# Optimization experiments

Measured on AMD Instinct MI355X. Metric: run time of the kernel, lower is better.

The kernel has to match this reference:

```python
import jax, jax.numpy as jnp
import numpy as np

# hidden irreps: 16x0e + 8x1o (dim 40); key/query: 8x0e + 4x1o (dim 24)
M0, M1 = 16, 8
K0, K1 = 8, 4
NB, HID = 16, 64       # radial basis size, radial MLP hidden
MAX_R = 2.0
NLAYERS = 2
SQ3 = 3.0 ** 0.5
N_NODES, N_EDGES = 8192, 131072


def _split(x, m0, m1):
    # [N, m0 + 3*m1] -> scalars [N,m0], vectors [N,m1,3]
    return x[:, :m0], x[:, m0:m0 + 3 * m1].reshape(x.shape[0], m1, 3)


def _lin(x, W0, W1, m0, m1):
    # e3nn o3.Linear: per-l block matmul with 1/sqrt(fan_in) norm
    s, v = _split(x, m0, m1)
    so = (s @ W0) * (m0 ** -0.5)
    vo = jnp.einsum('nui,uw->nwi', v, W1) * (m1 ** -0.5)
    return jnp.concatenate([so, vo.reshape(x.shape[0], -1)], axis=1)


def _radial(emb, W1, W2):
    # e3nn FullyConnectedNet [NB -> HID -> numel], no bias, 1/sqrt(fan_in)
    h = jax.nn.silu((emb @ W1) * (NB ** -0.5))
    return (h @ W2) * (HID ** -0.5)


def _fctp(s, v, y1, w, mo0, mo1):
    # FullyConnectedTensorProduct (hidden x sh(0e+1o) -> mo0 x0e + mo1 x1o)
    # with per-edge weights w. Y_0 = 1 under 'component' normalization.
    # Paths (in order of the weight slices):
    #   0e x 0e -> 0e,  0e x 1o -> 1o,  1o x 0e -> 1o,  1o x 1o -> 0e
    En, m0 = s.shape
    m1 = v.shape[1]
    i = 0
    W1 = w[:, i:i + m0 * mo0].reshape(En, m0, mo0); i += m0 * mo0
    W2 = w[:, i:i + m0 * mo1].reshape(En, m0, mo1); i += m0 * mo1
    W3 = w[:, i:i + m1 * mo1].reshape(En, m1, mo1); i += m1 * mo1
    W4 = w[:, i:i + m1 * mo0].reshape(En, m1, mo0)
    fan = float(m0 + m1)  # total mul1*mul2 feeding each output irrep
    vy = jnp.einsum('eui,ei->eu', v, y1) / SQ3  # w3j(1,1,0) = delta/sqrt3
    out_s = (jnp.einsum('eu,euw->ew', s, W1)
             + jnp.einsum('eu,euw->ew', vy, W4)) * (fan ** -0.5)
    out_v = (jnp.einsum('eu,ek,euw->ewk', s, y1, W2) / SQ3
             + jnp.einsum('eui,euw->ewi', v, W3)) * (SQ3 * fan ** -0.5)
    return out_s, out_v


def _edge_embed(d):
    # soft_one_hot_linspace(basis='gaussian', cutoff=True) * sqrt(NB)
    vals = jnp.linspace(0.0, MAX_R, NB + 2)[1:-1]
    step = MAX_R / (NB + 1)
    diff = (d[:, None] - vals) / step
    return (jnp.exp(-diff * diff) / 1.12) * (NB ** 0.5)


def _soft_unit_step(x):
    xs = jnp.maximum(x, 1e-9)
    return jnp.where(x > 0.0, jnp.exp(-1.0 / xs), 0.0)


def _layer(x, pos, src, dst, hq0, hq1, fck1, fck2, fcv1, fcv2, dot0, dot1):
    Nn = x.shape[0]
    vec = pos[src] - pos[dst]
    d = jnp.sqrt(jnp.sum(vec * vec, -1) + 1e-24)
    emb = _edge_embed(d)
    cutoff = _soft_unit_step(10.0 * (1.0 - d / MAX_R))
    y1 = SQ3 * vec / d[:, None]  # l=1 spherical harmonic, 'component' norm
    q = _lin(x, hq0, hq1, M0, M1)
    fs, fv = _split(x[src], M0, M1)
    ks_, kv_ = _fctp(fs, fv, y1, _radial(emb, fck1, fck2), K0, K1)
    vs_, vv_ = _fctp(fs, fv, y1, _radial(emb, fcv1, fcv2), M0, M1)
    qs, qv = _split(q[dst], K0, K1)
    fan = float(K0 * K0 + K1 * K1)
    logits = (jnp.einsum('eu,ev,uv->e', qs, ks_, dot0)
              + jnp.einsum('eui,evi,uv->e', qv, kv_, dot1) / SQ3) * (fan ** -0.5)
    mx = jax.ops.segment_max(logits, dst, num_segments=Nn)
    mx = jnp.where(jnp.isfinite(mx), mx, 0.0)
    ex = cutoff * jnp.exp(logits - mx[dst])
    z = jax.ops.segment_sum(ex, dst, num_segments=Nn)
    z = jnp.where(z == 0.0, 1.0, z)
    alpha = ex / z[dst]
    wgt = jnp.sqrt(jax.nn.relu(alpha) + 1e-12)
    val = jnp.concatenate([vs_, vv_.reshape(vs_.shape[0], -1)], axis=1)
    return jax.ops.segment_sum(wgt[:, None] * val, dst, num_segments=Nn)


def setup_inputs() -> dict:
    key = jax.random.key(0)
    ks = jax.random.split(key, 20)
    rn = lambda k, s: jax.random.normal(k, s, jnp.float32)
    f = rn(ks[0], (N_NODES, 40))
    pos = jax.random.uniform(ks[1], (N_NODES, 3), jnp.float32)
    src = jax.random.randint(ks[2], (N_EDGES,), 0, N_NODES, jnp.int32)
    off = jax.random.randint(ks[3], (N_EDGES,), 1, N_NODES, jnp.int32)
    dst = ((src + off) % N_NODES).astype(jnp.int32)  # no self-loops (loop=False)
    L = NLAYERS
    return dict(
        f=f, pos=pos,
        lin_in0=rn(ks[4], (16, 16)), lin_in1=rn(ks[5], (8, 8)),
        hq0=rn(ks[6], (L, 16, 8)), hq1=rn(ks[7], (L, 8, 4)),
        fck1=rn(ks[8], (L, 16, 64)), fck2=rn(ks[9], (L, 64, 288)),
        fcv1=rn(ks[10], (L, 16, 64)), fcv2=rn(ks[11], (L, 64, 576)),
        dot0=rn(ks[12], (L, 8, 8)), dot1=rn(ks[13], (L, 4, 4)),
        rb0=rn(ks[14], (16, 8)), rb1=rn(ks[15], (8, 4)),
        re0=rn(ks[16], (16, 8)), re1=rn(ks[17], (8, 4)),
        edge_src=src, edge_dst=dst,
    )


def reference(f, pos, lin_in0, lin_in1, hq0, hq1, fck1, fck2, fcv1, fcv2,
              dot0, dot1, rb0, rb1, re0, re1, edge_src, edge_dst):
    x = _lin(f, lin_in0, lin_in1, M0, M1)
    for l in range(NLAYERS):
        x = x + _layer(x, pos, edge_src, edge_dst, hq0[l], hq1[l],
                       fck1[l], fck2[l], fcv1[l], fcv2[l], dot0[l], dot1[l])
    b = _lin(x, rb0, rb1, M0, M1)
    eta = _lin(x, re0, re1, M0, M1)
    return b, eta
```

## Files before the change

### kernel.cpp

```cpp
#include <hip/hip_runtime.h>
#include <hip/hip_bf16.h>
#include <math.h>

#define DEV __device__ __forceinline__

typedef __attribute__((ext_vector_type(4))) float f32x4;
typedef __attribute__((ext_vector_type(8))) __bf16 bf16x8;

constexpr int N_CONST = 8192;
constexpr int E_CONST = 131072;

constexpr float SQ3F     = 1.7320508075688772f;
constexpr float INV_SQ3F = 0.57735026918962576f;
constexpr float FAN_TP   = 0.20412414523193150f;
constexpr float FAN_TP_V = 0.35355339059327373f;
constexpr float FAN_DOT  = 0.11180339887498949f;
constexpr float INV16SQ  = 0.25f;
constexpr float INV8SQ   = 0.35355339059327373f;
constexpr float HID_SC   = 0.125f;

enum : int {
  OFF_LIN0 = 0,
  OFF_LIN1 = OFF_LIN0 + 256,
  OFF_HQ0  = OFF_LIN1 + 64,
  OFF_HQ1  = OFF_HQ0 + 256,
  OFF_FCK1 = OFF_HQ1 + 64,
  OFF_FCK2 = OFF_FCK1 + 2048,
  OFF_FCV1 = OFF_FCK2 + 36864,
  OFF_FCV2 = OFF_FCV1 + 2048,
  OFF_DOT0 = OFF_FCV2 + 73728,
  OFF_DOT1 = OFF_DOT0 + 128,
  OFF_RB0  = OFF_DOT1 + 32,
  OFF_RB1  = OFF_RB0 + 128,
  OFF_RE0  = OFF_RB1 + 32,
  OFF_RE1  = OFF_RE0 + 128,
  OFF_F    = OFF_RE1 + 32,
  OFF_POS  = OFF_F + N_CONST * 40,
  OFF_X    = OFF_POS + N_CONST * 3,
  OFF_Q    = OFF_X + N_CONST * 40,
  OFF_MX   = OFF_Q + N_CONST * 20,
  OFF_Z    = OFF_MX + N_CONST,
  OFF_AGG  = OFF_Z + N_CONST,
  OFF_LOGIT= OFF_AGG + N_CONST * 40,
  OFF_CUT  = OFF_LOGIT + E_CONST,
  OFF_EX   = OFF_CUT + E_CONST,
  OFF_FLAG = OFF_EX + E_CONST,
  OFF_WT   = (OFF_FLAG + 7) & ~3,
  OFF_WTK  = OFF_WT + 36864,
};

__global__ void k_detect(const unsigned int* __restrict__ words, int* __restrict__ flag) {
  if (blockIdx.x != 0 || threadIdx.x != 0) return;
  int cnt = 0;
  for (int i = 0; i < 512; ++i) {
    unsigned b = (words[i] >> 8) & 0x7Fu;
    cnt += (b >= 0x3Au && b <= 0x43u) ? 1 : 0;
  }
  *flag = (cnt > 256) ? 1 : 0;
}

struct CvtArgs {
  const void* src[16];
  int n[16];
  int off[16];
};

template <bool BF>
__global__ void k_cvt(CvtArgs a, float* __restrict__ ws, const int* __restrict__ flag) {
  if ((*flag != 0) != BF) return;
  int tid = blockIdx.x * blockDim.x + threadIdx.x;
  int stride = gridDim.x * blockDim.x;
  for (int arr = 0; arr < 16; ++arr) {
    float* dst = ws + a.off[arr];
    int n = a.n[arr];
    if (BF) {
      const __hip_bfloat16* s = (const __hip_bfloat16*)a.src[arr];
      for (int i = tid; i < n; i += stride) dst[i] = __bfloat162float(s[i]);
    } else {
      const float* s = (const float*)a.src[arr];
      for (int i = tid; i < n; i += stride) dst[i] = s[i];
    }
  }
}

DEV unsigned short f2bf(float f) {
  unsigned int u = __float_as_uint(f);
  u = u + 0x7FFFu + ((u >> 16) & 1u);
  return (unsigned short)(u >> 16);
}

DEV void atomicMaxF(float* addr, float val) {
  unsigned int* ai = (unsigned int*)addr;
  unsigned int old = *ai;
  while (__uint_as_float(old) < val) {
    unsigned int assumed = old;
    old = atomicCAS(ai, assumed, __float_as_uint(val));
    if (old == assumed) break;
  }
}

template <int MO0, int MO1>
DEV void lin_apply(const float* __restrict__ in40, const float* __restrict__ W0,
                   const float* __restrict__ W1, float* __restrict__ out) {
#pragma unroll
  for (int j = 0; j < MO0; ++j) {
    float a = 0.f;
#pragma unroll
    for (int i = 0; i < 16; ++i) a += in40[i] * W0[i * MO0 + j];
    out[j] = a * INV16SQ;
  }
#pragma unroll
  for (int w = 0; w < MO1; ++w) {
    float a0 = 0.f, a1 = 0.f, a2 = 0.f;
#pragma unroll
    for (int u = 0; u < 8; ++u) {
      float wt = W1[u * MO1 + w];
      a0 += in40[16 + u * 3 + 0] * wt;
      a1 += in40[16 + u * 3 + 1] * wt;
      a2 += in40[16 + u * 3 + 2] * wt;
    }
    out[MO0 + w * 3 + 0] = a0 * INV8SQ;
    out[MO0 + w * 3 + 1] = a1 * INV8SQ;
    out[MO0 + w * 3 + 2] = a2 * INV8SQ;
  }
}

DEV void edge_emb(float d, float emb[16]) {
#pragma unroll
  for (int i = 0; i < 16; ++i) {
    float c = (2.0f * (i + 1)) / 17.0f;
    float df = (d - c) * (17.0f * 0.5f);
    emb[i] = __expf(-df * df) * (4.0f / 1.12f);
  }
}

DEV void radial_hidden16(const float* __restrict__ W1, const float emb[16],
                         int wv, float h[16]) {
#pragma unroll 1
  for (int i = 0; i < 16; ++i) {
    float a = 0.f;
#pragma unroll
    for (int j = 0; j < 16; ++j) a += emb[j] * W1[j * 64 + wv * 16 + i];
    a *= INV16SQ;
    float sig = 1.0f / (1.0f + __expf(-a));
    h[i] = a * sig * HID_SC;
  }
}

DEV void pack16(unsigned short* __restrict__ dst, const float h[16]) {
  unsigned int hw[8];
#pragma unroll
  for (int i = 0; i < 8; ++i)
    hw[i] = (unsigned int)f2bf(h[2 * i]) | ((unsigned int)f2bf(h[2 * i + 1]) << 16);
  uint4 w0 = {hw[0], hw[1], hw[2], hw[3]};
  uint4 w1 = {hw[4], hw[5], hw[6], hw[7]};
  *(uint4*)(dst) = w0;
  *(uint4*)(dst + 8) = w1;
}

DEV f32x4 gemm2_lds(const unsigned short* __restrict__ wb, int c, int g,
                    bf16x8 a0, bf16x8 a1) {
  const f32x4 zero4 = {0.f, 0.f, 0.f, 0.f};
  int s0 = g ^ (c & 7);
  bf16x8 b0 = __builtin_bit_cast(bf16x8, *(const uint4*)(wb + c * 64 + s0 * 8));
  bf16x8 b1 = __builtin_bit_cast(bf16x8, *(const uint4*)(wb + c * 64 + (s0 ^ 4) * 8));
  f32x4 acc = __builtin_amdgcn_mfma_f32_16x16x32_bf16(a0, b0, zero4, 0, 0, 0);
  return __builtin_amdgcn_mfma_f32_16x16x32_bf16(a1, b1, acc, 0, 0, 0);
}

__global__ void k_wt(const float* __restrict__ fcv2, unsigned short* __restrict__ wt) {
  int tid = blockIdx.x * blockDim.x + threadIdx.x;
  if (tid >= 2 * 36864) return;
  int l = tid / 36864;
  int r = tid - l * 36864;
  int T = r >> 10;
  int w = r & 1023;
  int c = w >> 6;
  int q = w & 63;
  int slot = (q >> 3) ^ (c & 7);
  int k = slot * 8 + (q & 7);
  wt[tid] = f2bf(fcv2[l * 36864 + k * 576 + T * 16 + c]);
}

__global__ void k_wtk(const float* __restrict__ fck2, unsigned short* __restrict__ wtk) {
  int tid = blockIdx.x * blockDim.x + threadIdx.x;
  if (tid >= 2 * 18432) return;
  int l = tid / 18432;
  int r = tid - l * 18432;
  int T = r >> 10;
  int w = r & 1023;
  int c = w >> 6;
  int q = w & 63;
  int slot = (q >> 3) ^ (c & 7);
  int k = slot * 8 + (q & 7);
  wtk[tid] = f2bf(fck2[l * 18432 + k * 288 + T * 16 + c]);
}

__global__ void k_lin_in(const float* __restrict__ f, const float* __restrict__ W0,
                         const float* __restrict__ W1, float* __restrict__ x, int N) {
  int n = blockIdx.x * blockDim.x + threadIdx.x;
  if (n >= N) return;
  lin_apply<16, 8>(f + n * 40, W0, W1, x + n * 40);
}

__global__ void k_q(const float* __restrict__ x, const float* __restrict__ W0,
                    const float* __restrict__ W1, float* __restrict__ q, int N) {
  int n = blockIdx.x * blockDim.x + threadIdx.x;
  if (n >= N) return;
  lin_apply<8, 4>(x + n * 40, W0, W1, q + n * 20);
}

__global__ void k_init(float* __restrict__ mx, float* __restrict__ z,
                       float* __restrict__ agg, int N) {
  int i = blockIdx.x * blockDim.x + threadIdx.x;
  if (i < N * 40) agg[i] = 0.f;
  if (i < N) { mx[i] = -INFINITY; z[i] = 0.f; }
}

__global__ void k_update(float* __restrict__ x, const float* __restrict__ agg, int n) {
  int i = blockIdx.x * blockDim.x + threadIdx.x;
  if (i < n) x[i] += agg[i];
}

__global__ void k_edge_ex(const int* __restrict__ dstv, const float* __restrict__ logit,
                          const float* __restrict__ cutb, const float* __restrict__ mx,
                          float* __restrict__ ex, float* __restrict__ z, int E) {
  int e = blockIdx.x * blockDim.x + threadIdx.x;
  if (e >= E) return;
  int t = dstv[e];
  float m = mx[t];
  if (m == -INFINITY) m = 0.f;
  float v = cutb[e] * __expf(logit[e] - m);
  ex[e] = v;
  atomicAdd(&z[t], v);
}

__global__ void __launch_bounds__(256)
k_edge_k(const float* __restrict__ pos, const float* __restrict__ x,
         const float* __restrict__ q,
         const float* __restrict__ fck1, const unsigned short* __restrict__ wtk,
         const float* __restrict__ dot0, const float* __restrict__ dot1,
         const int* __restrict__ srcv, const int* __restrict__ dstv,
         float* __restrict__ logit, float* __restrict__ cutb,
         float* __restrict__ mx, int E) {
  __shared__ alignas(16) unsigned short h_lds[64 * 72];
  __shared__ alignas(16) unsigned short wbuf[2 * 2 * 1024];
  __shared__ float fS[48][64];
  __shared__ float y1A[64][4];
  __shared__ float qdA[64][8];
  __shared__ float qvA[64][12];
  __shared__ int dstA[64];

  const int tid = threadIdx.x;
  const int wv = __builtin_amdgcn_readfirstlane(tid >> 6);
  const int lane = tid & 63;
  const int e0 = blockIdx.x * 64;
  const int eL = e0 + lane;
  const bool valid = eL < E;
  const bool ldr = (wv < 2);

  uint4 pre0, pre1;
  if (ldr) {
    const unsigned short* gs = wtk + wv * 1024 + lane * 8;
    pre0 = *(const uint4*)(gs);
    pre1 = *(const uint4*)(gs + 512);
  }

  int s = valid ? srcv[eL] : 0, t = valid ? dstv[eL] : 0;

  float y1v[3], d;
  {
    float vx = pos[s * 3 + 0] - pos[t * 3 + 0];
    float vy_ = pos[s * 3 + 1] - pos[t * 3 + 1];
    float vz = pos[s * 3 + 2] - pos[t * 3 + 2];
    d = sqrtf(vx * vx + vy_ * vy_ + vz * vz + 1e-24f);
    float inv = SQ3F / d;
    y1v[0] = vx * inv; y1v[1] = vy_ * inv; y1v[2] = vz * inv;
  }
  float emb[16];
  edge_emb(d, emb);
  {
    float h[16];
    radial_hidden16(fck1, emb, wv, h);
    pack16(&h_lds[lane * 72 + 16 * wv], h);
  }

  if (wv == 0) {
    const float* xs = x + s * 40;
    float fvl[24];
#pragma unroll
    for (int i = 0; i < 16; ++i) fS[i][lane] = xs[i];
#pragma unroll
    for (int i = 0; i < 24; ++i) { fvl[i] = xs[16 + i]; fS[16 + i][lane] = fvl[i]; }
#pragma unroll
    for (int u = 0; u < 8; ++u)
      fS[40 + u][lane] = (fvl[u * 3] * y1v[0] + fvl[u * 3 + 1] * y1v[1] +
                          fvl[u * 3 + 2] * y1v[2]) * INV_SQ3F;
    y1A[lane][0] = y1v[0]; y1A[lane][1] = y1v[1]; y1A[lane][2] = y1v[2];
    dstA[lane] = t;
    if (valid) {
      float uu = 10.0f * (1.0f - 0.5f * d);
      cutb[eL] = (uu > 0.f) ? __expf(-1.0f / fmaxf(uu, 1e-9f)) : 0.f;
    }
    const float* qd_ = q + t * 20;
    float qs_[8], qv_[12];
#pragma unroll
    for (int u = 0; u < 8; ++u) qs_[u] = qd_[u];
#pragma unroll
    for (int i = 0; i < 12; ++i) qv_[i] = qd_[8 + i];
#pragma unroll
    for (int v = 0; v < 8; ++v) {
      float a = 0.f;
#pragma unroll
      for (int u = 0; u < 8; ++u) a += qs_[u] * dot0[u * 8 + v];
      qdA[lane][v] = a * (FAN_DOT * FAN_TP);
    }
#pragma unroll
    for (int v = 0; v < 4; ++v)
#pragma unroll
      for (int i = 0; i < 3; ++i) {
        float a = 0.f;
#pragma unroll
        for (int u = 0; u < 4; ++u) a += qv_[u * 3 + i] * dot1[u * 4 + v];
        qvA[lane][v * 3 + i] = a * (FAN_DOT * INV_SQ3F);
      }
  }
  if (ldr) {
    unsigned short* wd = wbuf + wv * 1024 + lane * 8;
    *(uint4*)(wd) = pre0;
    *(uint4*)(wd + 512) = pre1;
  }
  __syncthreads();

  const int c = lane & 15, g = lane >> 4;
  const int erow = 16 * wv + 4 * g;

  bf16x8 a0 = __builtin_bit_cast(bf16x8, *(const uint4*)&h_lds[(16 * wv + c) * 72 + 8 * g]);
  bf16x8 a1 = __builtin_bit_cast(bf16x8, *(const uint4*)&h_lds[(16 * wv + c) * 72 + 32 + 8 * g]);

  float ksp[4] = {0.f, 0.f, 0.f, 0.f};
  float a2p[4] = {0.f, 0.f, 0.f, 0.f};
  float a3p[4][3] = {{0.f}};

#pragma unroll 1
  for (int p = 0; p < 9; ++p) {
    uint4 nb0, nb1;
    const bool hasNext = (p < 8) && ldr;
    if (hasNext) {
      const unsigned short* gs = wtk + (2 * (p + 1) + wv) * 1024 + lane * 8;
      nb0 = *(const uint4*)(gs);
      nb1 = *(const uint4*)(gs + 512);
    }
    const unsigned short* wb = wbuf + (p & 1) * 2048;
#pragma unroll
    for (int t2 = 0; t2 < 2; ++t2) {
      int T = 2 * p + t2;
      f32x4 acc = gemm2_lds(wb + t2 * 1024, c, g, a0, a1);
      if (T < 8) {
        int u = 2 * T + (c >> 3);
#pragma unroll
        for (int j = 0; j < 4; ++j) ksp[j] += fS[u][erow + j] * acc[j];
      } else if (T < 12) {
        int u = 4 * (T - 8) + (c >> 2);
#pragma unroll
        for (int j = 0; j < 4; ++j) a2p[j] += fS[u][erow + j] * acc[j];
      } else if (T < 14) {
        int u = 4 * (T - 12) + (c >> 2);
#pragma unroll
        for (int j = 0; j < 4; ++j)
#pragma unroll
          for (int i = 0; i < 3; ++i) a3p[j][i] += fS[16 + u * 3 + i][erow + j] * acc[j];
      } else {
        int u = 2 * (T - 14) + (c >> 3);
#pragma unroll
        for (int j = 0; j < 4; ++j) ksp[j] += fS[40 + u][erow + j] * acc[j];
      }
    }
    if (hasNext) {
      unsigned short* wd = wbuf + ((p + 1) & 1) * 2048 + wv * 1024 + lane * 8;
      *(uint4*)(wd) = nb0;
      *(uint4*)(wd + 512) = nb1;
    }
    __syncthreads();
  }

  float ksf[4], a2f[4], a3f[4][3];
#pragma unroll
  for (int j = 0; j < 4; ++j) ksf[j] = ksp[j] + __shfl_xor(ksp[j], 8);
#pragma unroll
  for (int j = 0; j < 4; ++j) {
    float v = a2p[j] + __shfl_xor(a2p[j], 4);
    a2f[j] = v + __shfl_xor(v, 8);
  }
#pragma unroll
  for (int j = 0; j < 4; ++j)
#pragma unroll
    for (int i = 0; i < 3; ++i) {
      float v = a3p[j][i] + __shfl_xor(a3p[j][i], 4);
      a3f[j][i] = v + __shfl_xor(v, 8);
    }

  float lgp[4];
#pragma unroll
  for (int j = 0; j < 4; ++j) {
    float a = 0.f;
    int er = erow + j;
    if (c < 8) {
      a = ksf[j] * qdA[er][c];
    } else if (c < 12) {
      int w = c - 8;
#pragma unroll
      for (int i = 0; i < 3; ++i)
        a += (a2f[j] * y1A[er][i] * FAN_TP + a3f[j][i] * FAN_TP_V) * qvA[er][w * 3 + i];
    }
    lgp[j] = a;
  }
#pragma unroll
  for (int j = 0; j < 4; ++j) {
    lgp[j] += __shfl_xor(lgp[j], 1);
    lgp[j] += __shfl_xor(lgp[j], 2);
    lgp[j] += __shfl_xor(lgp[j], 4);
    lgp[j] += __shfl_xor(lgp[j], 8);
  }
  if (c == 0) {
#pragma unroll
    for (int j = 0; j < 4; ++j) {
      int ee = e0 + erow + j;
      if (ee < E) {
        logit[ee] = lgp[j];
        atomicMaxF(&mx[dstA[erow + j]], lgp[j]);
      }
    }
  }
}

__global__ void __launch_bounds__(256)
k_edge_v(const float* __restrict__ pos, const float* __restrict__ x,
         const float* __restrict__ fcv1, const unsigned short* __restrict__ wtv,
         const int* __restrict__ srcv, const int* __restrict__ dstv,
         const float* __restrict__ ex, const float* __restrict__ z,
         float* __restrict__ agg, int E) {
  __shared__ alignas(16) unsigned short h_lds[64 * 72];
  __shared__ alignas(16) unsigned short wbuf[2 * 4 * 1024];
  __shared__ float fS[48][64];
  __shared__ float y1A[64][4];
  __shared__ float wgtA[64];
  __shared__ int dstA[64];

  const int tid = threadIdx.x;
  const int wv = __builtin_amdgcn_readfirstlane(tid >> 6);
  const int lane = tid & 63;
  const int e0 = blockIdx.x * 64;
  const int eL = e0 + lane;
  const bool valid = eL < E;

  uint4 pre0, pre1;
  {
    const unsigned short* gs = wtv + wv * 1024 + lane * 8;
    pre0 = *(const uint4*)(gs);
    pre1 = *(const uint4*)(gs + 512);
  }

  int s = valid ? srcv[eL] : 0, t = valid ? dstv[eL] : 0;

  float y1v[3], d;
  {
    float vx = pos[s * 3 + 0] - pos[t * 3 + 0];
    float vy_ = pos[s * 3 + 1] - pos[t * 3 + 1];
    float vz = pos[s * 3 + 2] - pos[t * 3 + 2];
    d = sqrtf(vx * vx + vy_ * vy_ + vz * vz + 1e-24f);
    float inv = SQ3F / d;
    y1v[0] = vx * inv; y1v[1] = vy_ * inv; y1v[2] = vz * inv;
  }
  float emb[16];
  edge_emb(d, emb);
  {
    float h[16];
    radial_hidden16(fcv1, emb, wv, h);
    pack16(&h_lds[lane * 72 + 16 * wv], h);
  }

  if (wv == 0) {
    const float* xs = x + s * 40;
    float fvl[24];
#pragma unroll
    for (int i = 0; i < 16; ++i) fS[i][lane] = xs[i];
#pragma unroll
    for (int i = 0; i < 24; ++i) { fvl[i] = xs[16 + i]; fS[16 + i][lane] = fvl[i]; }
#pragma unroll
    for (int u = 0; u < 8; ++u)
      fS[40 + u][lane] = (fvl[u * 3] * y1v[0] + fvl[u * 3 + 1] * y1v[1] +
                          fvl[u * 3 + 2] * y1v[2]) * INV_SQ3F;
    y1A[lane][0] = y1v[0]; y1A[lane][1] = y1v[1]; y1A[lane][2] = y1v[2];
    dstA[lane] = t;
    float zz = z[t];
    zz = (zz == 0.f) ? 1.f : zz;
    float alpha = (valid ? ex[eL] : 0.f) / zz;
    wgtA[lane] = sqrtf(alpha + 1e-12f);
  }
  {
    unsigned short* wd = wbuf + wv * 1024 + lane * 8;
    *(uint4*)(wd) = pre0;
    *(uint4*)(wd + 512) = pre1;
  }
  __syncthreads();

  const int c = lane & 15, g = lane >> 4;
  const int erow = 16 * wv + 4 * g;

  bf16x8 a0 = __builtin_bit_cast(bf16x8, *(const uint4*)&h_lds[(16 * wv + c) * 72 + 8 * g]);
  bf16x8 a1 = __builtin_bit_cast(bf16x8, *(const uint4*)&h_lds[(16 * wv + c) * 72 + 32 + 8 * g]);

  float vs[4] = {0.f, 0.f, 0.f, 0.f};
  float b2[4] = {0.f, 0.f, 0.f, 0.f};
  float b3[4][3] = {{0.f}};

#pragma unroll 1
  for (int p = 0; p < 9; ++p) {
    uint4 nb0, nb1;
    const bool hasNext = (p < 8);
    if (hasNext) {
      const unsigned short* gs = wtv + (4 * (p + 1) + wv) * 1024 + lane * 8;
      nb0 = *(const uint4*)(gs);
      nb1 = *(const uint4*)(gs + 512);
    }
    const unsigned short* wb = wbuf + (p & 1) * 4096;
#pragma unroll
    for (int t2 = 0; t2 < 4; ++t2) {
      int T = 4 * p + t2;
      f32x4 acc = gemm2_lds(wb + t2 * 1024, c, g, a0, a1);
      if (T < 16) {
#pragma unroll
        for (int j = 0; j < 4; ++j) vs[j] += fS[T][erow + j] * acc[j];
      } else if (T < 24) {
        int u = 2 * (T - 16) + (c >> 3);
#pragma unroll
        for (int j = 0; j < 4; ++j) b2[j] += fS[u][erow + j] * acc[j];
      } else if (T < 28) {
        int u = 2 * (T - 24) + (c >> 3);
#pragma unroll
        for (int j = 0; j < 4; ++j)
#pragma unroll
          for (int i = 0; i < 3; ++i) b3[j][i] += fS[16 + u * 3 + i][erow + j] * acc[j];
      } else {
#pragma unroll
        for (int j = 0; j < 4; ++j) vs[j] += fS[40 + (T - 28)][erow + j] * acc[j];
      }
    }
    if (hasNext) {
      unsigned short* wd = wbuf + ((p + 1) & 1) * 4096 + wv * 1024 + lane * 8;
      *(uint4*)(wd) = nb0;
      *(uint4*)(wd + 512) = nb1;
    }
    __syncthreads();
  }

#pragma unroll
  for (int j = 0; j < 4; ++j) b2[j] += __shfl_xor(b2[j], 8);
#pragma unroll
  for (int j = 0; j < 4; ++j)
#pragma unroll
    for (int i = 0; i < 3; ++i) b3[j][i] += __shfl_xor(b3[j][i], 8);

#pragma unroll
  for (int j = 0; j < 4; ++j) {
    int er = erow + j;
    int ee = e0 + er;
    if (ee >= E) continue;
    float w = wgtA[er];
    float* at = agg + dstA[er] * 40;
    atomicAdd(&at[c], w * vs[j] * FAN_TP);
    if (c < 8) {
#pragma unroll
      for (int i = 0; i < 2; ++i) {
        float v = b2[j] * y1A[er][i] * FAN_TP + b3[j][i] * FAN_TP_V;
        atomicAdd(&at[16 + c * 3 + i], w * v);
      }
    } else {
      float v = b2[j] * y1A[er][2] * FAN_TP + b3[j][2] * FAN_TP_V;
      atomicAdd(&at[16 + (c - 8) * 3 + 2], w * v);
    }
  }
}

template <bool BF>
__global__ void k_out(const float* __restrict__ x, const float* __restrict__ rb0,
                      const float* __restrict__ rb1, const float* __restrict__ re0,
                      const float* __restrict__ re1, void* __restrict__ out, int N,
                      const int* __restrict__ flag) {
  if ((*flag != 0) != BF) return;
  int n = blockIdx.x * blockDim.x + threadIdx.x;
  if (n >= N) return;
  float b[20], eta[20];
  lin_apply<8, 4>(x + n * 40, rb0, rb1, b);
  lin_apply<8, 4>(x + n * 40, re0, re1, eta);
  if (BF) {
    __hip_bfloat16* o = (__hip_bfloat16*)out;
#pragma unroll
    for (int j = 0; j < 20; ++j) o[n * 20 + j] = __float2bfloat16(b[j]);
#pragma unroll
    for (int j = 0; j < 20; ++j) o[N * 20 + n * 20 + j] = __float2bfloat16(eta[j]);
  } else {
    float* o = (float*)out;
#pragma unroll
    for (int j = 0; j < 20; ++j) o[n * 20 + j] = b[j];
#pragma unroll
    for (int j = 0; j < 20; ++j) o[N * 20 + n * 20 + j] = eta[j];
  }
}

extern "C" void kernel_launch(void* const* d_in, const int* in_sizes, int n_in,
                              void* d_out, int out_size, void* d_ws, size_t ws_size,
                              hipStream_t stream) {
  float* ws = (float*)d_ws;
  const int N = in_sizes[0] / 40;
  const int E = in_sizes[16];
  const int* src = (const int*)d_in[16];
  const int* dst = (const int*)d_in[17];
  int* flag = (int*)(ws + OFF_FLAG);
  unsigned short* wtv = (unsigned short*)(ws + OFF_WT);
  unsigned short* wtk = (unsigned short*)(ws + OFF_WTK);

  k_detect<<<1, 64, 0, stream>>>((const unsigned int*)d_in[0], flag);

  CvtArgs ca;
  const int order[16] = {2, 3, 4, 5, 6, 7, 8, 9, 10, 11, 12, 13, 14, 15, 0, 1};
  const int offs[16] = {OFF_LIN0, OFF_LIN1, OFF_HQ0, OFF_HQ1, OFF_FCK1, OFF_FCK2,
                        OFF_FCV1, OFF_FCV2, OFF_DOT0, OFF_DOT1, OFF_RB0, OFF_RB1,
                        OFF_RE0, OFF_RE1, OFF_F, OFF_POS};
  for (int i = 0; i < 16; ++i) {
    ca.src[i] = d_in[order[i]];
    ca.n[i] = in_sizes[order[i]];
    ca.off[i] = offs[i];
  }
  k_cvt<false><<<512, 256, 0, stream>>>(ca, ws, flag);
  k_cvt<true><<<512, 256, 0, stream>>>(ca, ws, flag);
  k_wt<<<(2 * 36864 + 255) / 256, 256, 0, stream>>>(ws + OFF_FCV2, wtv);
  k_wtk<<<(2 * 18432 + 255) / 256, 256, 0, stream>>>(ws + OFF_FCK2, wtk);

  float* x = ws + OFF_X;
  float* q = ws + OFF_Q;
  float* mx = ws + OFF_MX;
  float* z = ws + OFF_Z;
  float* agg = ws + OFF_AGG;
  float* logit = ws + OFF_LOGIT;
  float* cutb = ws + OFF_CUT;
  float* exb = ws + OFF_EX;
  const float* pos = ws + OFF_POS;

  const int nodeBlocks = (N + 255) / 256;
  const int vecBlocks = (N * 40 + 255) / 256;
  const int edgeBlocks = (E + 255) / 256;
  const int eb64 = (E + 63) / 64;

  k_lin_in<<<nodeBlocks, 256, 0, stream>>>(ws + OFF_F, ws + OFF_LIN0, ws + OFF_LIN1, x, N);

  for (int l = 0; l < 2; ++l) {
    k_init<<<vecBlocks, 256, 0, stream>>>(mx, z, agg, N);
    k_q<<<nodeBlocks, 256, 0, stream>>>(x, ws + OFF_HQ0 + l * 128, ws + OFF_HQ1 + l * 32, q, N);
    k_edge_k<<<eb64, 256, 0, stream>>>(
        pos, x, q, ws + OFF_FCK1 + l * 1024, wtk + l * 18432,
        ws + OFF_DOT0 + l * 64, ws + OFF_DOT1 + l * 16, src, dst, logit, cutb, mx, E);
    k_edge_ex<<<edgeBlocks, 256, 0, stream>>>(dst, logit, cutb, mx, exb, z, E);
    k_edge_v<<<eb64, 256, 0, stream>>>(
        pos, x, ws + OFF_FCV1 + l * 1024, wtv + l * 36864, src, dst, exb, z, agg, E);
    k_update<<<vecBlocks, 256, 0, stream>>>(x, agg, N * 40);
  }

  k_out<false><<<nodeBlocks, 256, 0, stream>>>(x, ws + OFF_RB0, ws + OFF_RB1,
                                               ws + OFF_RE0, ws + OFF_RE1, d_out, N, flag);
  k_out<true><<<nodeBlocks, 256, 0, stream>>>(x, ws + OFF_RB0, ws + OFF_RB1,
                                              ws + OFF_RE0, ws + OFF_RE1, d_out, N, flag);
}
```

Baseline: 286.0 us.

## Restructure value-edge MFMA tiling, stage scatter in LDS, fuse residual update

k_edge_v's work split changes: each wave now handles two 16-edge row blocks and half of the weight tiles, chosen by a tileOf mapping. Each B-tile LDS load therefore feeds two MFMAs. The two output halves are combined in LDS (reusing wbuf) and then scattered with coalesced atomicAdds, 40 contiguous floats per edge spread over 4 threads, instead of strided per-lane atomics. The residual update kernel is folded into the next layer's q kernel and into the output kernel, which removes a launch and one pass over x. fS reads are also vectorised as f32x4 loads in both edge kernels. The costs are extra barriers, LDS traffic for the reduction, and more registers per wave.

```diff
diff --git a/kernel.cpp b/kernel.cpp
--- a/kernel.cpp
+++ b/kernel.cpp
@@ -158,14 +158,12 @@
   *(uint4*)(dst + 8) = w1;
 }
 
-DEV f32x4 gemm2_lds(const unsigned short* __restrict__ wb, int c, int g,
-                    bf16x8 a0, bf16x8 a1) {
-  const f32x4 zero4 = {0.f, 0.f, 0.f, 0.f};
-  int s0 = g ^ (c & 7);
-  bf16x8 b0 = __builtin_bit_cast(bf16x8, *(const uint4*)(wb + c * 64 + s0 * 8));
-  bf16x8 b1 = __builtin_bit_cast(bf16x8, *(const uint4*)(wb + c * 64 + (s0 ^ 4) * 8));
-  f32x4 acc = __builtin_amdgcn_mfma_f32_16x16x32_bf16(a0, b0, zero4, 0, 0, 0);
-  return __builtin_amdgcn_mfma_f32_16x16x32_bf16(a1, b1, acc, 0, 0, 0);
+DEV int tileOf(int i, int nh) {
+  int b = i, o = 8;
+  if (i >= 8)  { b += 8; o -= 4; }
+  if (i >= 12) { b += 4; o -= 2; }
+  if (i >= 14) { b += 2; o += 2; }
+  return b + nh * o;
 }
 
 __global__ void k_wt(const float* __restrict__ fcv2, unsigned short* __restrict__ wt) {
@@ -203,11 +201,23 @@
   lin_apply<16, 8>(f + n * 40, W0, W1, x + n * 40);
 }
 
-__global__ void k_q(const float* __restrict__ x, const float* __restrict__ W0,
-                    const float* __restrict__ W1, float* __restrict__ q, int N) {
+__global__ void k_qup(float* __restrict__ x, const float* __restrict__ agg,
+                      const float* __restrict__ W0, const float* __restrict__ W1,
+                      float* __restrict__ q, int N, int doAdd) {
   int n = blockIdx.x * blockDim.x + threadIdx.x;
   if (n >= N) return;
-  lin_apply<8, 4>(x + n * 40, W0, W1, q + n * 20);
+  float xn[40];
+  if (doAdd) {
+#pragma unroll
+    for (int i = 0; i < 40; ++i) {
+      xn[i] = x[n * 40 + i] + agg[n * 40 + i];
+      x[n * 40 + i] = xn[i];
+    }
+  } else {
+#pragma unroll
+    for (int i = 0; i < 40; ++i) xn[i] = x[n * 40 + i];
+  }
+  lin_apply<8, 4>(xn, W0, W1, q + n * 20);
 }
 
 __global__ void k_init(float* __restrict__ mx, float* __restrict__ z,
@@ -215,11 +225,6 @@
   int i = blockIdx.x * blockDim.x + threadIdx.x;
   if (i < N * 40) agg[i] = 0.f;
   if (i < N) { mx[i] = -INFINITY; z[i] = 0.f; }
-}
-
-__global__ void k_update(float* __restrict__ x, const float* __restrict__ agg, int n) {
-  int i = blockIdx.x * blockDim.x + threadIdx.x;
-  if (i < n) x[i] += agg[i];
 }
 
 __global__ void k_edge_ex(const int* __restrict__ dstv, const float* __restrict__ logit,
@@ -334,6 +339,7 @@
 
   const int c = lane & 15, g = lane >> 4;
   const int erow = 16 * wv + 4 * g;
+  const f32x4 zero4 = {0.f, 0.f, 0.f, 0.f};
 
   bf16x8 a0 = __builtin_bit_cast(bf16x8, *(const uint4*)&h_lds[(16 * wv + c) * 72 + 8 * g]);
   bf16x8 a1 = __builtin_bit_cast(bf16x8, *(const uint4*)&h_lds[(16 * wv + c) * 72 + 32 + 8 * g]);
@@ -355,25 +361,35 @@
 #pragma unroll
     for (int t2 = 0; t2 < 2; ++t2) {
       int T = 2 * p + t2;
-      f32x4 acc = gemm2_lds(wb + t2 * 1024, c, g, a0, a1);
+      int s0 = g ^ (c & 7);
+      const unsigned short* wtile = wb + t2 * 1024 + c * 64;
+      bf16x8 b0 = __builtin_bit_cast(bf16x8, *(const uint4*)(wtile + s0 * 8));
+      bf16x8 b1 = __builtin_bit_cast(bf16x8, *(const uint4*)(wtile + (s0 ^ 4) * 8));
+      f32x4 acc = __builtin_amdgcn_mfma_f32_16x16x32_bf16(a0, b0, zero4, 0, 0, 0);
+      acc = __builtin_amdgcn_mfma_f32_16x16x32_bf16(a1, b1, acc, 0, 0, 0);
       if (T < 8) {
         int u = 2 * T + (c >> 3);
-#pragma unroll
-        for (int j = 0; j < 4; ++j) ksp[j] += fS[u][erow + j] * acc[j];
+        f32x4 f4 = *(const f32x4*)&fS[u][erow];
+#pragma unroll
+        for (int j = 0; j < 4; ++j) ksp[j] += f4[j] * acc[j];
       } else if (T < 12) {
         int u = 4 * (T - 8) + (c >> 2);
-#pragma unroll
-        for (int j = 0; j < 4; ++j) a2p[j] += fS[u][erow + j] * acc[j];
+        f32x4 f4 = *(const f32x4*)&fS[u][erow];
+#pragma unroll
+        for (int j = 0; j < 4; ++j) a2p[j] += f4[j] * acc[j];
       } else if (T < 14) {
         int u = 4 * (T - 12) + (c >> 2);
 #pragma unroll
-        for (int j = 0; j < 4; ++j)
-#pragma unroll
-          for (int i = 0; i < 3; ++i) a3p[j][i] += fS[16 + u * 3 + i][erow + j] * acc[j];
+        for (int i = 0; i < 3; ++i) {
+          f32x4 f4 = *(const f32x4*)&fS[16 + u * 3 + i][erow];
+#pragma unroll
+          for (int j = 0; j < 4; ++j) a3p[j][i] += f4[j] * acc[j];
+        }
       } else {
         int u = 2 * (T - 14) + (c >> 3);
-#pragma unroll
-        for (int j = 0; j < 4; ++j) ksp[j] += fS[40 + u][erow + j] * acc[j];
+        f32x4 f4 = *(const f32x4*)&fS[40 + u][erow];
+#pragma unroll
+        for (int j = 0; j < 4; ++j) ksp[j] += f4[j] * acc[j];
       }
     }
     if (hasNext) {
@@ -450,13 +466,16 @@
   const int tid = threadIdx.x;
   const int wv = __builtin_amdgcn_readfirstlane(tid >> 6);
   const int lane = tid & 63;
+  const int wp = wv & 1;
+  const int nh = wv >> 1;
   const int e0 = blockIdx.x * 64;
   const int eL = e0 + lane;
   const bool valid = eL < E;
 
   uint4 pre0, pre1;
   {
-    const unsigned short* gs = wtv + wv * 1024 + lane * 8;
+    int T = tileOf(wv & 1, wv >> 1);
+    const unsigned short* gs = wtv + T * 1024 + lane * 8;
     pre0 = *(const uint4*)(gs);
     pre1 = *(const uint4*)(gs + 512);
   }
@@ -506,45 +525,63 @@
   __syncthreads();
 
   const int c = lane & 15, g = lane >> 4;
-  const int erow = 16 * wv + 4 * g;
-
-  bf16x8 a0 = __builtin_bit_cast(bf16x8, *(const uint4*)&h_lds[(16 * wv + c) * 72 + 8 * g]);
-  bf16x8 a1 = __builtin_bit_cast(bf16x8, *(const uint4*)&h_lds[(16 * wv + c) * 72 + 32 + 8 * g]);
-
-  float vs[4] = {0.f, 0.f, 0.f, 0.f};
-  float b2[4] = {0.f, 0.f, 0.f, 0.f};
-  float b3[4][3] = {{0.f}};
+  const f32x4 zero4 = {0.f, 0.f, 0.f, 0.f};
+
+  bf16x8 aV[2][2];
+#pragma unroll
+  for (int m = 0; m < 2; ++m)
+#pragma unroll
+    for (int ks = 0; ks < 2; ++ks)
+      aV[m][ks] = __builtin_bit_cast(
+          bf16x8, *(const uint4*)&h_lds[(32 * wp + 16 * m + c) * 72 + 32 * ks + 8 * g]);
+
+  float vs[2][4] = {{0.f}}, b2[2][4] = {{0.f}}, b3[2][4][3] = {{{0.f}}};
 
 #pragma unroll 1
   for (int p = 0; p < 9; ++p) {
     uint4 nb0, nb1;
     const bool hasNext = (p < 8);
     if (hasNext) {
-      const unsigned short* gs = wtv + (4 * (p + 1) + wv) * 1024 + lane * 8;
+      int T = tileOf(2 * (p + 1) + (wv & 1), wv >> 1);
+      const unsigned short* gs = wtv + T * 1024 + lane * 8;
       nb0 = *(const uint4*)(gs);
       nb1 = *(const uint4*)(gs + 512);
     }
-    const unsigned short* wb = wbuf + (p & 1) * 4096;
-#pragma unroll
-    for (int t2 = 0; t2 < 4; ++t2) {
-      int T = 4 * p + t2;
-      f32x4 acc = gemm2_lds(wb + t2 * 1024, c, g, a0, a1);
-      if (T < 16) {
-#pragma unroll
-        for (int j = 0; j < 4; ++j) vs[j] += fS[T][erow + j] * acc[j];
-      } else if (T < 24) {
-        int u = 2 * (T - 16) + (c >> 3);
-#pragma unroll
-        for (int j = 0; j < 4; ++j) b2[j] += fS[u][erow + j] * acc[j];
-      } else if (T < 28) {
-        int u = 2 * (T - 24) + (c >> 3);
-#pragma unroll
-        for (int j = 0; j < 4; ++j)
-#pragma unroll
-          for (int i = 0; i < 3; ++i) b3[j][i] += fS[16 + u * 3 + i][erow + j] * acc[j];
-      } else {
-#pragma unroll
-        for (int j = 0; j < 4; ++j) vs[j] += fS[40 + (T - 28)][erow + j] * acc[j];
+    const unsigned short* wb = wbuf + (p & 1) * 4096 + 2 * nh * 1024;
+#pragma unroll
+    for (int t2 = 0; t2 < 2; ++t2) {
+      int T = tileOf(2 * p + t2, nh);
+      int s0 = g ^ (c & 7);
+      const unsigned short* wtile = wb + t2 * 1024 + c * 64;
+      bf16x8 b0 = __builtin_bit_cast(bf16x8, *(const uint4*)(wtile + s0 * 8));
+      bf16x8 b1 = __builtin_bit_cast(bf16x8, *(const uint4*)(wtile + (s0 ^ 4) * 8));
+#pragma unroll
+      for (int m = 0; m < 2; ++m) {
+        f32x4 acc = __builtin_amdgcn_mfma_f32_16x16x32_bf16(aV[m][0], b0, zero4, 0, 0, 0);
+        acc = __builtin_amdgcn_mfma_f32_16x16x32_bf16(aV[m][1], b1, acc, 0, 0, 0);
+        const int rb = 32 * wp + 16 * m + 4 * g;
+        if (T < 16) {
+          f32x4 f4 = *(const f32x4*)&fS[T][rb];
+#pragma unroll
+          for (int j = 0; j < 4; ++j) vs[m][j] += f4[j] * acc[j];
+        } else if (T < 24) {
+          int u = 2 * (T - 16) + (c >> 3);
+          f32x4 f4 = *(const f32x4*)&fS[u][rb];
+#pragma unroll
+          for (int j = 0; j < 4; ++j) b2[m][j] += f4[j] * acc[j];
+        } else if (T < 28) {
+          int u = 2 * (T - 24) + (c >> 3);
+#pragma unroll
+          for (int i = 0; i < 3; ++i) {
+            f32x4 f4 = *(const f32x4*)&fS[16 + u * 3 + i][rb];
+#pragma unroll
+            for (int j = 0; j < 4; ++j) b3[m][j][i] += f4[j] * acc[j];
+          }
+        } else {
+          f32x4 f4 = *(const f32x4*)&fS[40 + (T - 28)][rb];
+#pragma unroll
+          for (int j = 0; j < 4; ++j) vs[m][j] += f4[j] * acc[j];
+        }
       }
     }
     if (hasNext) {
@@ -556,44 +593,81 @@
   }
 
 #pragma unroll
-  for (int j = 0; j < 4; ++j) b2[j] += __shfl_xor(b2[j], 8);
-#pragma unroll
-  for (int j = 0; j < 4; ++j)
-#pragma unroll
-    for (int i = 0; i < 3; ++i) b3[j][i] += __shfl_xor(b3[j][i], 8);
-
-#pragma unroll
-  for (int j = 0; j < 4; ++j) {
-    int er = erow + j;
-    int ee = e0 + er;
-    if (ee >= E) continue;
-    float w = wgtA[er];
-    float* at = agg + dstA[er] * 40;
-    atomicAdd(&at[c], w * vs[j] * FAN_TP);
-    if (c < 8) {
-#pragma unroll
-      for (int i = 0; i < 2; ++i) {
-        float v = b2[j] * y1A[er][i] * FAN_TP + b3[j][i] * FAN_TP_V;
-        atomicAdd(&at[16 + c * 3 + i], w * v);
+  for (int m = 0; m < 2; ++m) {
+#pragma unroll
+    for (int j = 0; j < 4; ++j) b2[m][j] += __shfl_xor(b2[m][j], 8);
+#pragma unroll
+    for (int j = 0; j < 4; ++j)
+#pragma unroll
+      for (int i = 0; i < 3; ++i) b3[m][j][i] += __shfl_xor(b3[m][j][i], 8);
+  }
+
+  float* accF = (float*)wbuf;
+  if (nh == 0) {
+#pragma unroll
+    for (int m = 0; m < 2; ++m)
+#pragma unroll
+      for (int j = 0; j < 4; ++j) {
+        int er = 32 * wp + 16 * m + 4 * g + j;
+        accF[er * 40 + c] = vs[m][j] * FAN_TP;
+        if (c < 8) {
+          accF[er * 40 + 16 + 3 * c + 0] = b2[m][j] * y1A[er][0] * FAN_TP + b3[m][j][0] * FAN_TP_V;
+          accF[er * 40 + 16 + 3 * c + 1] = b2[m][j] * y1A[er][1] * FAN_TP + b3[m][j][1] * FAN_TP_V;
+        } else {
+          accF[er * 40 + 16 + 3 * (c - 8) + 2] =
+              b2[m][j] * y1A[er][2] * FAN_TP + b3[m][j][2] * FAN_TP_V;
+        }
       }
-    } else {
-      float v = b2[j] * y1A[er][2] * FAN_TP + b3[j][2] * FAN_TP_V;
-      atomicAdd(&at[16 + (c - 8) * 3 + 2], w * v);
+  }
+  __syncthreads();
+  if (nh == 1) {
+#pragma unroll
+    for (int m = 0; m < 2; ++m)
+#pragma unroll
+      for (int j = 0; j < 4; ++j) {
+        int er = 32 * wp + 16 * m + 4 * g + j;
+        accF[er * 40 + c] += vs[m][j] * FAN_TP;
+        if (c < 8) {
+          accF[er * 40 + 16 + 3 * c + 0] += b2[m][j] * y1A[er][0] * FAN_TP + b3[m][j][0] * FAN_TP_V;
+          accF[er * 40 + 16 + 3 * c + 1] += b2[m][j] * y1A[er][1] * FAN_TP + b3[m][j][1] * FAN_TP_V;
+        } else {
+          accF[er * 40 + 16 + 3 * (c - 8) + 2] +=
+              b2[m][j] * y1A[er][2] * FAN_TP + b3[m][j][2] * FAN_TP_V;
+        }
+      }
+  }
+  __syncthreads();
+
+  {
+    int ep = tid >> 2, p4 = tid & 3;
+    int ee = e0 + ep;
+    if (ee < E) {
+      float w = wgtA[ep];
+      float* at = agg + dstA[ep] * 40;
+      const float* af = accF + ep * 40;
+#pragma unroll
+      for (int q2 = 0; q2 < 10; ++q2) {
+        int idx = p4 * 10 + q2;
+        atomicAdd(&at[idx], w * af[idx]);
+      }
     }
   }
 }
 
 template <bool BF>
-__global__ void k_out(const float* __restrict__ x, const float* __restrict__ rb0,
-                      const float* __restrict__ rb1, const float* __restrict__ re0,
-                      const float* __restrict__ re1, void* __restrict__ out, int N,
-                      const int* __restrict__ flag) {
+__global__ void k_out(const float* __restrict__ x, const float* __restrict__ agg,
+                      const float* __restrict__ rb0, const float* __restrict__ rb1,
+                      const float* __restrict__ re0, const float* __restrict__ re1,
+                      void* __restrict__ out, int N, const int* __restrict__ flag) {
   if ((*flag != 0) != BF) return;
   int n = blockIdx.x * blockDim.x + threadIdx.x;
   if (n >= N) return;
+  float xn[40];
+#pragma unroll
+  for (int i = 0; i < 40; ++i) xn[i] = x[n * 40 + i] + agg[n * 40 + i];
   float b[20], eta[20];
-  lin_apply<8, 4>(x + n * 40, rb0, rb1, b);
-  lin_apply<8, 4>(x + n * 40, re0, re1, eta);
+  lin_apply<8, 4>(xn, rb0, rb1, b);
+  lin_apply<8, 4>(xn, re0, re1, eta);
   if (BF) {
     __hip_bfloat16* o = (__hip_bfloat16*)out;
 #pragma unroll
@@ -656,19 +730,19 @@
   k_lin_in<<<nodeBlocks, 256, 0, stream>>>(ws + OFF_F, ws + OFF_LIN0, ws + OFF_LIN1, x, N);
 
   for (int l = 0; l < 2; ++l) {
+    k_qup<<<nodeBlocks, 256, 0, stream>>>(x, agg, ws + OFF_HQ0 + l * 128,
+                                          ws + OFF_HQ1 + l * 32, q, N, l > 0 ? 1 : 0);
     k_init<<<vecBlocks, 256, 0, stream>>>(mx, z, agg, N);
-    k_q<<<nodeBlocks, 256, 0, stream>>>(x, ws + OFF_HQ0 + l * 128, ws + OFF_HQ1 + l * 32, q, N);
     k_edge_k<<<eb64, 256, 0, stream>>>(
         pos, x, q, ws + OFF_FCK1 + l * 1024, wtk + l * 18432,
         ws + OFF_DOT0 + l * 64, ws + OFF_DOT1 + l * 16, src, dst, logit, cutb, mx, E);
     k_edge_ex<<<edgeBlocks, 256, 0, stream>>>(dst, logit, cutb, mx, exb, z, E);
     k_edge_v<<<eb64, 256, 0, stream>>>(
         pos, x, ws + OFF_FCV1 + l * 1024, wtv + l * 36864, src, dst, exb, z, agg, E);
-    k_update<<<vecBlocks, 256, 0, stream>>>(x, agg, N * 40);
-  }
-
-  k_out<false><<<nodeBlocks, 256, 0, stream>>>(x, ws + OFF_RB0, ws + OFF_RB1,
+  }
+
+  k_out<false><<<nodeBlocks, 256, 0, stream>>>(x, agg, ws + OFF_RB0, ws + OFF_RB1,
                                                ws + OFF_RE0, ws + OFF_RE1, d_out, N, flag);
-  k_out<true><<<nodeBlocks, 256, 0, stream>>>(x, ws + OFF_RB0, ws + OFF_RB1,
+  k_out<true><<<nodeBlocks, 256, 0, stream>>>(x, agg, ws + OFF_RB0, ws + OFF_RB1,
                                               ws + OFF_RE0, ws + OFF_RE1, d_out, N, flag);
 }
```

Result: slower. 605.9 us (+111.9%).
